# Kernel optimization log

Hardware: AMD Instinct MI355X
Metric: run time of the kernel (lower is better)

The kernel has to match this reference:

```python
import jax, jax.numpy as jnp
import numpy as np

NEG_SLOPE = 0.2  # LeakyReLU slope
B, F_BAND, T = 32, 128, 2048
HID, NCLASS = 256, 64


def _corrcoef(m):
    # m: [..., n, k] -> correlation matrix between rows, [..., n, n] (torch.corrcoef semantics)
    m = m - m.mean(axis=-1, keepdims=True)
    c = jnp.einsum('...ik,...jk->...ij', m, m)
    d = jnp.sqrt(jnp.clip(jnp.diagonal(c, axis1=-2, axis2=-1), 0.0, None))
    corr = c / (d[..., :, None] * d[..., None, :])
    return jnp.clip(corr, -1.0, 1.0)


def _leaky(x):
    return jnp.where(x >= 0, x, NEG_SLOPE * x)


def setup_inputs() -> dict:
    key = jax.random.key(0)
    ks = jax.random.split(key, 9)
    def lin(k, fin, fout):
        return jax.random.normal(k, (fin, fout), dtype=jnp.float32) / np.sqrt(fin)
    x = jax.random.normal(ks[0], (B, F_BAND, T), dtype=jnp.float32)
    return {
        'x': x,
        'W1': lin(ks[1], T, HID),      'b1': jnp.zeros((HID,), jnp.float32),
        'W2': lin(ks[2], HID, HID),    'b2': jnp.zeros((HID,), jnp.float32),
        'W3': lin(ks[3], HID, NCLASS), 'b3': jnp.zeros((NCLASS,), jnp.float32),
        'W4': lin(ks[4], NCLASS, NCLASS), 'b4': jnp.zeros((NCLASS,), jnp.float32),
    }


def reference(x, W1, b1, W2, b2, W3, b3, W4, b4):
    Bs, Fb, Tt = x.shape
    node = Fb
    step = node  # typeFeature=2 -> overlap=0
    A = len(range(0, Tt - node, step))  # number of time windows
    # windows: x[:, :, a*node:(a+1)*node] -> [B, A, F, node]
    xw = x[:, :, :A * node].reshape(Bs, Fb, A, node).transpose(0, 2, 1, 3)
    # torch.corrcoef(fi.T): rows = window-column index (node), variables over F bands
    adj = _corrcoef(jnp.swapaxes(xw, -1, -2))  # [B, A, node, node] == [B, A, F, F]
    adj = jnp.nan_to_num((adj + 1.0) * 0.5)
    # gnnBlock vectorized over all A windows (x broadcast along A). Dropout is eval-mode no-op.
    h = _leaky(jnp.einsum('banm,bmt->bant', adj, x) @ W1 + b1)    # [B,A,F,HID]
    h = _leaky(jnp.einsum('banm,bamh->banh', adj, h) @ W2 + b2)   # [B,A,F,HID]
    xa = _leaky(jnp.einsum('banm,bamh->banh', adj, h) @ W3 + b3)  # [B,A,F,C]
    # typeFeature==2 head: mean over nodes, corrcoef over windows, gc4
    xa = xa.mean(axis=2)         # [B, A, C]
    adj2 = _corrcoef(xa)         # [B, A, A]
    out = _leaky(jnp.einsum('bij,bjc->bic', adj2, xa) @ W4 + b4)  # [B, A, C]
    # max over dim=1; GradMultiply with grad_mul=1.0 is identity in fwd
    return out.max(axis=1)       # [B, C]
```

## Files before the change

### kernel.cpp

```cpp
#include <hip/hip_runtime.h>


typedef float f32x4 __attribute__((ext_vector_type(4)));
typedef __bf16 bf16x8 __attribute__((ext_vector_type(8)));
typedef unsigned short u16x4 __attribute__((ext_vector_type(4)));
typedef unsigned short u16x8 __attribute__((ext_vector_type(8)));

__device__ inline unsigned short f2b(float f) {
  unsigned int u = __float_as_uint(f);
  unsigned int r = u + 0x7fffu + ((u >> 16) & 1u);
  return (unsigned short)(r >> 16);
}
__device__ inline float leaky(float v) { return v >= 0.f ? v : 0.2f * v; }

#define SWZ(k, r) ((k) ^ (((r) & 7) << 3))

__global__ __launch_bounds__(256) void k_prep(const float* __restrict__ x,
                                              const float* __restrict__ W1,
                                              const float* __restrict__ W2,
                                              const float* __restrict__ W3,
                                              unsigned short* __restrict__ W1T,
                                              unsigned short* __restrict__ W2T,
                                              unsigned short* __restrict__ W3T,
                                              unsigned short* __restrict__ xT) {
  __shared__ float t[64][65];
  const int bid = blockIdx.x;
  const int tid = threadIdx.x;
  if (bid < 148) {
    const float* src;
    unsigned short* dst;
    int K, N, k0, n0;
    if (bid < 128) {
      src = W1; dst = W1T; K = 2048; N = 256;
      k0 = (bid >> 2) * 64; n0 = (bid & 3) * 64;
    } else if (bid < 144) {
      src = W2; dst = W2T; K = 256; N = 256;
      int i = bid - 128; k0 = (i >> 2) * 64; n0 = (i & 3) * 64;
    } else {
      src = W3; dst = W3T; K = 256; N = 64;
      int i = bid - 144; k0 = i * 64; n0 = 0;
    }
#pragma unroll
    for (int it = 0; it < 16; ++it) {
      int e = tid + it * 256, r = e >> 6, c = e & 63;
      t[r][c] = src[(size_t)(k0 + r) * N + n0 + c];
    }
    __syncthreads();
#pragma unroll
    for (int it = 0; it < 16; ++it) {
      int e = tid + it * 256, rr = e >> 6, cc = e & 63;
      dst[(size_t)(n0 + rr) * K + k0 + cc] = f2b(t[cc][rr]);
    }
  } else {
    int idx = bid - 148;
    int b = idx >> 6, rem = idx & 63;
    int tt = rem >> 1, ft = rem & 1;
    int t0 = tt * 64, f0 = ft * 64;
    const float* xb = x + ((size_t)b * 128 + f0) * 2048 + t0;
#pragma unroll
    for (int it = 0; it < 16; ++it) {
      int e = tid + it * 256, r = e >> 6, c = e & 63;
      t[r][c] = xb[(size_t)r * 2048 + c];
    }
    __syncthreads();
    unsigned short* dst = xT + ((size_t)b * 2048 + t0) * 128 + f0;
#pragma unroll
    for (int it = 0; it < 4; ++it) {
      int e = tid + it * 256, rr = e >> 4, c4 = (e & 15) * 4;
      u16x4 s;
#pragma unroll
      for (int q = 0; q < 4; ++q) s[q] = f2b(t[c4 + q][rr]);
      *(u16x4*)&dst[rr * 128 + c4] = s;
    }
  }
}

__global__ __launch_bounds__(512) void k_xw1(const float* __restrict__ x,
                                             const unsigned short* __restrict__ W1T,
                                             unsigned short* __restrict__ XW1T) {
  __shared__ __align__(16) unsigned short sX[2][64 * 64];
  const int tid = threadIdx.x;
  const int w = tid >> 6, lane = tid & 63;
  const int l15 = lane & 15, l4 = lane >> 4;
  const int bx = blockIdx.x;
  const int hid0 = (bx >> 1) * 64, f0 = (bx & 1) * 64;
  const int b = blockIdx.y;
  const float* xb = x + ((size_t)b * 128 + f0) * 2048;
  const int arow = hid0 + (w & 3) * 16 + l15;
  const int nb = (w >> 2) * 32;
  const int fr = tid >> 3, k8 = (tid & 7) * 8;

  f32x4 xr2[2];
  f32x4 acc[2] = {};

  auto LOADX = [&](int kb) {
    xr2[0] = *(const f32x4*)&xb[(size_t)fr * 2048 + kb * 64 + k8];
    xr2[1] = *(const f32x4*)&xb[(size_t)fr * 2048 + kb * 64 + k8 + 4];
  };
  auto STOREX = [&](int buf) {
    u16x8 s;
#pragma unroll
    for (int j = 0; j < 8; ++j) s[j] = f2b(xr2[j >> 2][j & 3]);
    *(u16x8*)&sX[buf][fr * 64 + SWZ(k8, fr)] = s;
  };

  LOADX(0);
  STOREX(0);
  __syncthreads();
  for (int kb = 0; kb < 32; ++kb) {
    if (kb < 31) LOADX(kb + 1);
    const int buf = kb & 1;
    bf16x8 af0 = *(const bf16x8*)&W1T[(size_t)arow * 2048 + kb * 64 + l4 * 8];
    bf16x8 af1 = *(const bf16x8*)&W1T[(size_t)arow * 2048 + kb * 64 + 32 + l4 * 8];
#pragma unroll
    for (int nt = 0; nt < 2; ++nt) {
      int br = nb + nt * 16 + l15;
      bf16x8 b0 = *(const bf16x8*)&sX[buf][br * 64 + SWZ(l4 * 8, br)];
      acc[nt] = __builtin_amdgcn_mfma_f32_16x16x32_bf16(af0, b0, acc[nt], 0, 0, 0);
    }
#pragma unroll
    for (int nt = 0; nt < 2; ++nt) {
      int br = nb + nt * 16 + l15;
      bf16x8 b1 = *(const bf16x8*)&sX[buf][br * 64 + SWZ(32 + l4 * 8, br)];
      acc[nt] = __builtin_amdgcn_mfma_f32_16x16x32_bf16(af1, b1, acc[nt], 0, 0, 0);
    }
    if (kb < 31) {
      STOREX(buf ^ 1);
      __syncthreads();
    }
  }
  unsigned short* dst = XW1T + (size_t)b * 256 * 128;
#pragma unroll
  for (int nt = 0; nt < 2; ++nt)
#pragma unroll
    for (int r = 0; r < 4; ++r) {
      int p = hid0 + (w & 3) * 16 + l4 * 4 + r;
      int f = f0 + nb + nt * 16 + l15;
      dst[p * 128 + f] = f2b(acc[nt][r]);
    }
}

__global__ __launch_bounds__(512, 4) void k_chain(
    const unsigned short* __restrict__ xT, const unsigned short* __restrict__ XW1T,
    const unsigned short* __restrict__ W2T, const unsigned short* __restrict__ W3T,
    const float* __restrict__ b1g, const float* __restrict__ b2g,
    const float* __restrict__ b3g, float* __restrict__ gXa) {
  __shared__ __align__(16) unsigned short R0[128 * 128];
  __shared__ __align__(16) unsigned short R1[128 * 128];
  __shared__ float fS[384];

  const int tid = threadIdx.x;
  const int w = tid >> 6, lane = tid & 63;
  const int l15 = lane & 15, l4 = lane >> 4;
  const int b = blockIdx.x / 15, a = blockIdx.x % 15;
  const int m0 = w * 16;

  const unsigned short* src = xT + ((size_t)b * 2048 + (size_t)a * 128) * 128;
#pragma unroll
  for (int it = 0; it < 4; ++it) {
    int tt = tid + it * 512;
    int j = tt >> 4, f8 = (tt & 15) * 8;
    *(u16x8*)&R1[j * 128 + SWZ(f8, j)] = *(const u16x8*)&src[j * 128 + f8];
  }
  __syncthreads();

  {
    f32x4 acc8[8] = {};
    f32x4 sacc = {};
    bf16x8 ones;
#pragma unroll
    for (int q = 0; q < 8; ++q) ones[q] = (__bf16)1.0f;
    __builtin_amdgcn_s_setprio(1);
#pragma unroll
    for (int ks = 0; ks < 4; ++ks) {
      int ar = m0 + l15;
      bf16x8 af = *(const bf16x8*)&R1[ar * 128 + SWZ(ks * 32 + l4 * 8, ar)];
      sacc = __builtin_amdgcn_mfma_f32_16x16x32_bf16(af, ones, sacc, 0, 0, 0);
#pragma unroll
      for (int nt = 0; nt < 8; ++nt) {
        int br = nt * 16 + l15;
        bf16x8 bf = *(const bf16x8*)&R1[br * 128 + SWZ(ks * 32 + l4 * 8, br)];
        acc8[nt] = __builtin_amdgcn_mfma_f32_16x16x32_bf16(af, bf, acc8[nt], 0, 0, 0);
      }
    }
    __builtin_amdgcn_s_setprio(0);
    if (l15 == 0) {
#pragma unroll
      for (int r = 0; r < 4; ++r) fS[m0 + l4 * 4 + r] = sacc[r];
    }
    __syncthreads();
    const float inv128 = 1.f / 128.f;
    float fcol[8];
#pragma unroll
    for (int nt = 0; nt < 8; ++nt) fcol[nt] = fS[nt * 16 + l15];
#pragma unroll
    for (int nt = 0; nt < 8; ++nt)
#pragma unroll
      for (int r = 0; r < 4; ++r) {
        int row = m0 + l4 * 4 + r, col = nt * 16 + l15;
        float c = acc8[nt][r] - sacc[r] * fcol[nt] * inv128;
        acc8[nt][r] = c;
        if (row == col) fS[128 + row] = c;
      }
    __syncthreads();
    if (tid < 128) {
      float d = fS[128 + tid];
      fS[256 + tid] = d > 0.f ? 1.f / sqrtf(d) : 0.f;
    }
    __syncthreads();
    float djv[8], div[4];
#pragma unroll
    for (int nt = 0; nt < 8; ++nt) djv[nt] = fS[256 + nt * 16 + l15];
#pragma unroll
    for (int r = 0; r < 4; ++r) div[r] = fS[256 + m0 + l4 * 4 + r];
#pragma unroll
    for (int nt = 0; nt < 8; ++nt)
#pragma unroll
      for (int r = 0; r < 4; ++r) {
        int row = m0 + l4 * 4 + r, col = nt * 16 + l15;
        float v = acc8[nt][r] * div[r] * djv[nt];
        v = fminf(1.f, fmaxf(-1.f, v));
        v = 0.5f * v + 0.5f;
        if (div[r] == 0.f || djv[nt] == 0.f) v = 0.f;
        R0[row * 128 + SWZ(col, row)] = f2b(v);
      }
  }
  bf16x8 afj[4];
#pragma unroll
  for (int ks = 0; ks < 4; ++ks)
    afj[ks] = *(const bf16x8*)&R0[(m0 + l15) * 128 + SWZ(ks * 32 + l4 * 8, m0 + l15)];
  __syncthreads();

  const unsigned short* XWb = XW1T + (size_t)b * 256 * 128;
#pragma unroll 1
  for (int half = 0; half < 2; ++half) {
    f32x4 acc[8] = {};
    __builtin_amdgcn_s_setprio(1);
#pragma unroll
    for (int ks = 0; ks < 4; ++ks)
#pragma unroll
      for (int nt = 0; nt < 8; ++nt) {
        bf16x8 bf = *(const bf16x8*)&XWb[(size_t)(half * 128 + nt * 16 + l15) * 128 + ks * 32 + l4 * 8];
        acc[nt] = __builtin_amdgcn_mfma_f32_16x16x32_bf16(afj[ks], bf, acc[nt], 0, 0, 0);
      }
    __builtin_amdgcn_s_setprio(0);
    unsigned short* Rd = half ? R1 : R0;
#pragma unroll
    for (int nt = 0; nt < 8; ++nt) {
      float bias = b1g[half * 128 + nt * 16 + l15];
#pragma unroll
      for (int r = 0; r < 4; ++r) {
        int row = m0 + l4 * 4 + r, col = nt * 16 + l15;
        Rd[row * 128 + SWZ(col, row)] = f2b(leaky(acc[nt][r] + bias));
      }
    }
  }
  __syncthreads();

  {
    f32x4 u2[2][8] = {};
    __builtin_amdgcn_s_setprio(1);
#pragma unroll
    for (int ks = 0; ks < 8; ++ks) {
      bf16x8 a0 = *(const bf16x8*)&W2T[(size_t)(w * 32 + l15) * 256 + ks * 32 + l4 * 8];
      bf16x8 a1 = *(const bf16x8*)&W2T[(size_t)(w * 32 + 16 + l15) * 256 + ks * 32 + l4 * 8];
      const unsigned short* Rs = (ks < 4) ? R0 : R1;
      int kk = (ks & 3) * 32 + l4 * 8;
#pragma unroll
      for (int nt = 0; nt < 8; ++nt) {
        int br = nt * 16 + l15;
        bf16x8 bf = *(const bf16x8*)&Rs[br * 128 + SWZ(kk, br)];
        u2[0][nt] = __builtin_amdgcn_mfma_f32_16x16x32_bf16(a0, bf, u2[0][nt], 0, 0, 0);
        u2[1][nt] = __builtin_amdgcn_mfma_f32_16x16x32_bf16(a1, bf, u2[1][nt], 0, 0, 0);
      }
    }
    __builtin_amdgcn_s_setprio(0);
    __syncthreads();
#pragma unroll
    for (int mt = 0; mt < 2; ++mt)
#pragma unroll
      for (int nt = 0; nt < 8; ++nt)
#pragma unroll
        for (int r = 0; r < 4; ++r) {
          int grow = w * 32 + mt * 16 + l4 * 4 + r;
          int col = nt * 16 + l15;
          unsigned short* Rd = (grow < 128) ? R0 : R1;
          int lr = grow & 127;
          Rd[lr * 128 + SWZ(col, lr)] = f2b(u2[mt][nt][r]);
        }
  }
  __syncthreads();

  f32x4 h2acc[8];
#pragma unroll
  for (int nt = 0; nt < 8; ++nt) h2acc[nt] = f32x4{0.f, 0.f, 0.f, 0.f};
  __builtin_amdgcn_s_setprio(1);
#pragma unroll
  for (int ks = 0; ks < 4; ++ks)
#pragma unroll
    for (int nt = 0; nt < 8; ++nt) {
      int br = nt * 16 + l15;
      bf16x8 bf = *(const bf16x8*)&R0[br * 128 + SWZ(ks * 32 + l4 * 8, br)];
      h2acc[nt] = __builtin_amdgcn_mfma_f32_16x16x32_bf16(afj[ks], bf, h2acc[nt], 0, 0, 0);
    }
  __builtin_amdgcn_s_setprio(0);
  __syncthreads();
#pragma unroll
  for (int nt = 0; nt < 8; ++nt) {
    float bias = b2g[nt * 16 + l15];
#pragma unroll
    for (int r = 0; r < 4; ++r) {
      int row = m0 + l4 * 4 + r, col = nt * 16 + l15;
      R0[row * 128 + SWZ(col, row)] = f2b(leaky(h2acc[nt][r] + bias));
    }
  }
  __syncthreads();

  f32x4 u3[4] = {};
  const int mrow = (w >> 1) * 16, ntb = (w & 1) * 4;
  __builtin_amdgcn_s_setprio(1);
#pragma unroll
  for (int ks = 0; ks < 4; ++ks) {
    bf16x8 a3 = *(const bf16x8*)&W3T[(size_t)(mrow + l15) * 256 + ks * 32 + l4 * 8];
#pragma unroll
    for (int nti = 0; nti < 4; ++nti) {
      int br = (ntb + nti) * 16 + l15;
      bf16x8 bf = *(const bf16x8*)&R0[br * 128 + SWZ(ks * 32 + l4 * 8, br)];
      u3[nti] = __builtin_amdgcn_mfma_f32_16x16x32_bf16(a3, bf, u3[nti], 0, 0, 0);
    }
  }
#pragma unroll
  for (int nt = 0; nt < 8; ++nt) h2acc[nt] = f32x4{0.f, 0.f, 0.f, 0.f};
#pragma unroll
  for (int ks = 0; ks < 4; ++ks)
#pragma unroll
    for (int nt = 0; nt < 8; ++nt) {
      int br = nt * 16 + l15;
      bf16x8 bf = *(const bf16x8*)&R1[br * 128 + SWZ(ks * 32 + l4 * 8, br)];
      h2acc[nt] = __builtin_amdgcn_mfma_f32_16x16x32_bf16(afj[ks], bf, h2acc[nt], 0, 0, 0);
    }
  __builtin_amdgcn_s_setprio(0);
  __syncthreads();
#pragma unroll
  for (int nt = 0; nt < 8; ++nt) {
    float bias = b2g[128 + nt * 16 + l15];
#pragma unroll
    for (int r = 0; r < 4; ++r) {
      int row = m0 + l4 * 4 + r, col = nt * 16 + l15;
      R1[row * 128 + SWZ(col, row)] = f2b(leaky(h2acc[nt][r] + bias));
    }
  }
  __syncthreads();

  __builtin_amdgcn_s_setprio(1);
#pragma unroll
  for (int ks = 0; ks < 4; ++ks) {
    bf16x8 a3 = *(const bf16x8*)&W3T[(size_t)(mrow + l15) * 256 + 128 + ks * 32 + l4 * 8];
#pragma unroll
    for (int nti = 0; nti < 4; ++nti) {
      int br = (ntb + nti) * 16 + l15;
      bf16x8 bf = *(const bf16x8*)&R1[br * 128 + SWZ(ks * 32 + l4 * 8, br)];
      u3[nti] = __builtin_amdgcn_mfma_f32_16x16x32_bf16(a3, bf, u3[nti], 0, 0, 0);
    }
  }
  __builtin_amdgcn_s_setprio(0);
  __syncthreads();
#pragma unroll
  for (int nti = 0; nti < 4; ++nti)
#pragma unroll
    for (int r = 0; r < 4; ++r) {
      int grow = mrow + l4 * 4 + r;
      int col = (ntb + nti) * 16 + l15;
      R0[grow * 128 + SWZ(col, grow)] = f2b(u3[nti][r]);
    }
  __syncthreads();

  {
    f32x4 xacc[4] = {};
    __builtin_amdgcn_s_setprio(1);
#pragma unroll
    for (int ks = 0; ks < 4; ++ks)
#pragma unroll
      for (int nt = 0; nt < 4; ++nt) {
        int br = nt * 16 + l15;
        bf16x8 bf = *(const bf16x8*)&R0[br * 128 + SWZ(ks * 32 + l4 * 8, br)];
        xacc[nt] = __builtin_amdgcn_mfma_f32_16x16x32_bf16(afj[ks], bf, xacc[nt], 0, 0, 0);
      }
    __builtin_amdgcn_s_setprio(0);
    float* xaf = reinterpret_cast<float*>(R1);
#pragma unroll
    for (int nt = 0; nt < 4; ++nt) {
      float bias = b3g[nt * 16 + l15];
#pragma unroll
      for (int r = 0; r < 4; ++r) {
        int row = m0 + l4 * 4 + r, col = nt * 16 + l15;
        xaf[row * 64 + col] = leaky(xacc[nt][r] + bias);
      }
    }
  }
  __syncthreads();
  {
    const float* xaf = reinterpret_cast<const float*>(R1);
    float* part = reinterpret_cast<float*>(R0);
    int c = tid & 63, g = tid >> 6;
    float s = 0.f;
#pragma unroll
    for (int i = 0; i < 16; ++i) s += xaf[(g * 16 + i) * 64 + c];
    part[g * 64 + c] = s;
    __syncthreads();
    if (tid < 64) {
      float tt = 0.f;
#pragma unroll
      for (int gg = 0; gg < 8; ++gg) tt += part[gg * 64 + tid];
      gXa[((size_t)b * 15 + a) * 64 + tid] = tt * (1.f / 128.f);
    }
  }
}

__global__ __launch_bounds__(256) void k_head(const float* __restrict__ gXa,
                                              const float* __restrict__ W4,
                                              const float* __restrict__ b4,
                                              float* __restrict__ out) {
  __shared__ float xb[15 * 64];
  __shared__ float c2[15 * 16];
  __shared__ float mu[15];
  __shared__ float dinv[15];
  __shared__ float yy[15 * 64];
  __shared__ float zz[15 * 64];
  const int b = blockIdx.x;
  const int tid = threadIdx.x;
  for (int e = tid; e < 960; e += 256) xb[e] = gXa[(size_t)b * 960 + e];
  __syncthreads();
  if (tid < 15) {
    float s = 0.f;
    for (int c = 0; c < 64; ++c) s += xb[tid * 64 + c];
    mu[tid] = s * (1.f / 64.f);
  }
  __syncthreads();
  if (tid < 225) {
    int p = tid / 15, q = tid % 15;
    float s = 0.f;
    for (int c = 0; c < 64; ++c)
      s += (xb[p * 64 + c] - mu[p]) * (xb[q * 64 + c] - mu[q]);
    c2[p * 16 + q] = s;
  }
  __syncthreads();
  if (tid < 15) {
    float d = c2[tid * 16 + tid];
    dinv[tid] = d > 0.f ? (1.f / sqrtf(d)) : 0.f;
  }
  __syncthreads();
  if (tid < 225) {
    int p = tid / 15, q = tid % 15;
    float v = c2[p * 16 + q] * dinv[p] * dinv[q];
    v = fminf(1.f, fmaxf(-1.f, v));
    if (dinv[p] == 0.f || dinv[q] == 0.f) v = 0.f;
    c2[p * 16 + q] = v;
  }
  __syncthreads();
  for (int e = tid; e < 960; e += 256) {
    int p = e >> 6, c = e & 63;
    float s = 0.f;
    for (int q = 0; q < 15; ++q) s += c2[p * 16 + q] * xb[q * 64 + c];
    yy[e] = s;
  }
  __syncthreads();
  for (int e = tid; e < 960; e += 256) {
    int p = e >> 6, c = e & 63;
    float s = b4[c];
    for (int k = 0; k < 64; ++k) s += yy[p * 64 + k] * W4[k * 64 + c];
    zz[e] = leaky(s);
  }
  __syncthreads();
  if (tid < 64) {
    float m = -INFINITY;
    for (int p = 0; p < 15; ++p) m = fmaxf(m, zz[p * 64 + tid]);
    out[(size_t)b * 64 + tid] = m;
  }
}

extern "C" void kernel_launch(void* const* d_in, const int* in_sizes, int n_in,
                              void* d_out, int out_size, void* d_ws, size_t ws_size,
                              hipStream_t stream) {
  const float* x  = (const float*)d_in[0];
  const float* W1 = (const float*)d_in[1];
  const float* b1 = (const float*)d_in[2];
  const float* W2 = (const float*)d_in[3];
  const float* b2 = (const float*)d_in[4];
  const float* W3 = (const float*)d_in[5];
  const float* b3 = (const float*)d_in[6];
  const float* W4 = (const float*)d_in[7];
  const float* b4 = (const float*)d_in[8];
  float* out = (float*)d_out;

  char* ws = (char*)d_ws;
  unsigned short* xT   = (unsigned short*)ws;
  unsigned short* XW1T = (unsigned short*)(ws + 16777216);
  unsigned short* W1T  = (unsigned short*)(ws + 18874368);
  unsigned short* W2T  = (unsigned short*)(ws + 19922944);
  unsigned short* W3T  = (unsigned short*)(ws + 20054016);
  float* gXa           = (float*)(ws + 20086784);

  k_prep<<<2196, 256, 0, stream>>>(x, W1, W2, W3, W1T, W2T, W3T, xT);
  dim3 gx(8, 32);
  k_xw1<<<gx, 512, 0, stream>>>(x, W1T, XW1T);
  k_chain<<<480, 512, 0, stream>>>(xT, XW1T, W2T, W3T, b1, b2, b3, gXa);
  k_head<<<32, 256, 0, stream>>>(gXa, W4, b4, out);
}
```

Baseline: 132.8 us.

## Fuse x transpose with XW1 GEMM, stage XW1 in LDS, reorder chain stages

```diff
diff --git a/kernel.cpp b/kernel.cpp
--- a/kernel.cpp
+++ b/kernel.cpp
@@ -3,7 +3,6 @@
 
 typedef float f32x4 __attribute__((ext_vector_type(4)));
 typedef __bf16 bf16x8 __attribute__((ext_vector_type(8)));
-typedef unsigned short u16x4 __attribute__((ext_vector_type(4)));
 typedef unsigned short u16x8 __attribute__((ext_vector_type(8)));
 
 __device__ inline unsigned short f2b(float f) {
@@ -15,129 +14,121 @@
 
 #define SWZ(k, r) ((k) ^ (((r) & 7) << 3))
 
-__global__ __launch_bounds__(256) void k_prep(const float* __restrict__ x,
-                                              const float* __restrict__ W1,
-                                              const float* __restrict__ W2,
-                                              const float* __restrict__ W3,
-                                              unsigned short* __restrict__ W1T,
-                                              unsigned short* __restrict__ W2T,
-                                              unsigned short* __restrict__ W3T,
-                                              unsigned short* __restrict__ xT) {
+__global__ __launch_bounds__(256) void k_prepw(const float* __restrict__ W1,
+                                               const float* __restrict__ W2,
+                                               const float* __restrict__ W3,
+                                               unsigned short* __restrict__ W1T,
+                                               unsigned short* __restrict__ W2T,
+                                               unsigned short* __restrict__ W3T) {
   __shared__ float t[64][65];
   const int bid = blockIdx.x;
   const int tid = threadIdx.x;
-  if (bid < 148) {
-    const float* src;
-    unsigned short* dst;
-    int K, N, k0, n0;
-    if (bid < 128) {
-      src = W1; dst = W1T; K = 2048; N = 256;
-      k0 = (bid >> 2) * 64; n0 = (bid & 3) * 64;
-    } else if (bid < 144) {
-      src = W2; dst = W2T; K = 256; N = 256;
-      int i = bid - 128; k0 = (i >> 2) * 64; n0 = (i & 3) * 64;
-    } else {
-      src = W3; dst = W3T; K = 256; N = 64;
-      int i = bid - 144; k0 = i * 64; n0 = 0;
-    }
-#pragma unroll
-    for (int it = 0; it < 16; ++it) {
-      int e = tid + it * 256, r = e >> 6, c = e & 63;
-      t[r][c] = src[(size_t)(k0 + r) * N + n0 + c];
-    }
+  const float* src;
+  unsigned short* dst;
+  int K, N, k0, n0;
+  if (bid < 128) {
+    src = W1; dst = W1T; K = 2048; N = 256;
+    k0 = (bid >> 2) * 64; n0 = (bid & 3) * 64;
+  } else if (bid < 144) {
+    src = W2; dst = W2T; K = 256; N = 256;
+    int i = bid - 128; k0 = (i >> 2) * 64; n0 = (i & 3) * 64;
+  } else {
+    src = W3; dst = W3T; K = 256; N = 64;
+    int i = bid - 144; k0 = i * 64; n0 = 0;
+  }
+#pragma unroll
+  for (int it = 0; it < 16; ++it) {
+    int e = tid + it * 256, r = e >> 6, c = e & 63;
+    t[r][c] = src[(size_t)(k0 + r) * N + n0 + c];
+  }
+  __syncthreads();
+#pragma unroll
+  for (int it = 0; it < 16; ++it) {
+    int e = tid + it * 256, rr = e >> 6, cc = e & 63;
+    dst[(size_t)(n0 + rr) * K + k0 + cc] = f2b(t[cc][rr]);
+  }
+}
+
+__global__ __launch_bounds__(512) void k_front(const float* __restrict__ x,
+                                               const unsigned short* __restrict__ W1T,
+                                               unsigned short* __restrict__ xT,
+                                               unsigned short* __restrict__ XW1T) {
+  __shared__ __align__(16) char ldsbuf[16896];
+  const int bid = blockIdx.x;
+  const int tid = threadIdx.x;
+  if (bid < 2048) {
+    float (*t)[65] = reinterpret_cast<float (*)[65]>(ldsbuf);
+    int b = bid >> 6, rem = bid & 63;
+    int t0 = (rem >> 1) * 64, f0 = (rem & 1) * 64;
+    const float* xb = x + ((size_t)b * 128 + f0) * 2048 + t0;
+    int r = tid >> 3, c8 = (tid & 7) * 8;
+    f32x4 v0 = *(const f32x4*)&xb[(size_t)r * 2048 + c8];
+    f32x4 v1 = *(const f32x4*)&xb[(size_t)r * 2048 + c8 + 4];
+    *(f32x4*)&t[r][c8] = v0;
+    *(f32x4*)&t[r][c8 + 4] = v1;
     __syncthreads();
-#pragma unroll
-    for (int it = 0; it < 16; ++it) {
-      int e = tid + it * 256, rr = e >> 6, cc = e & 63;
-      dst[(size_t)(n0 + rr) * K + k0 + cc] = f2b(t[cc][rr]);
-    }
+    u16x8 s;
+#pragma unroll
+    for (int q = 0; q < 8; ++q) s[q] = f2b(t[c8 + q][r]);
+    *(u16x8*)&xT[((size_t)b * 2048 + t0 + r) * 128 + f0 + c8] = s;
   } else {
-    int idx = bid - 148;
-    int b = idx >> 6, rem = idx & 63;
-    int tt = rem >> 1, ft = rem & 1;
-    int t0 = tt * 64, f0 = ft * 64;
-    const float* xb = x + ((size_t)b * 128 + f0) * 2048 + t0;
-#pragma unroll
-    for (int it = 0; it < 16; ++it) {
-      int e = tid + it * 256, r = e >> 6, c = e & 63;
-      t[r][c] = xb[(size_t)r * 2048 + c];
-    }
+    unsigned short (*sX)[64 * 64] = reinterpret_cast<unsigned short (*)[64 * 64]>(ldsbuf);
+    const int i = bid - 2048;
+    const int b = i >> 1, f0 = (i & 1) * 64;
+    const int w = tid >> 6, lane = tid & 63;
+    const int l15 = lane & 15, l4 = lane >> 4;
+    const float* xb = x + ((size_t)b * 128 + f0) * 2048;
+    const int fr = tid >> 3, k8 = (tid & 7) * 8;
+    f32x4 xr0, xr1;
+    f32x4 acc[2][4] = {};
+
+    auto LOADX = [&](int kb) {
+      xr0 = *(const f32x4*)&xb[(size_t)fr * 2048 + kb * 64 + k8];
+      xr1 = *(const f32x4*)&xb[(size_t)fr * 2048 + kb * 64 + k8 + 4];
+    };
+    auto STOREX = [&](int buf) {
+      u16x8 s;
+#pragma unroll
+      for (int q = 0; q < 8; ++q) s[q] = f2b(q < 4 ? xr0[q] : xr1[q - 4]);
+      *(u16x8*)&sX[buf][fr * 64 + SWZ(k8, fr)] = s;
+    };
+
+    LOADX(0);
+    STOREX(0);
     __syncthreads();
-    unsigned short* dst = xT + ((size_t)b * 2048 + t0) * 128 + f0;
-#pragma unroll
-    for (int it = 0; it < 4; ++it) {
-      int e = tid + it * 256, rr = e >> 4, c4 = (e & 15) * 4;
-      u16x4 s;
-#pragma unroll
-      for (int q = 0; q < 4; ++q) s[q] = f2b(t[c4 + q][rr]);
-      *(u16x4*)&dst[rr * 128 + c4] = s;
-    }
-  }
-}
-
-__global__ __launch_bounds__(512) void k_xw1(const float* __restrict__ x,
-                                             const unsigned short* __restrict__ W1T,
-                                             unsigned short* __restrict__ XW1T) {
-  __shared__ __align__(16) unsigned short sX[2][64 * 64];
-  const int tid = threadIdx.x;
-  const int w = tid >> 6, lane = tid & 63;
-  const int l15 = lane & 15, l4 = lane >> 4;
-  const int bx = blockIdx.x;
-  const int hid0 = (bx >> 1) * 64, f0 = (bx & 1) * 64;
-  const int b = blockIdx.y;
-  const float* xb = x + ((size_t)b * 128 + f0) * 2048;
-  const int arow = hid0 + (w & 3) * 16 + l15;
-  const int nb = (w >> 2) * 32;
-  const int fr = tid >> 3, k8 = (tid & 7) * 8;
-
-  f32x4 xr2[2];
-  f32x4 acc[2] = {};
-
-  auto LOADX = [&](int kb) {
-    xr2[0] = *(const f32x4*)&xb[(size_t)fr * 2048 + kb * 64 + k8];
-    xr2[1] = *(const f32x4*)&xb[(size_t)fr * 2048 + kb * 64 + k8 + 4];
-  };
-  auto STOREX = [&](int buf) {
-    u16x8 s;
-#pragma unroll
-    for (int j = 0; j < 8; ++j) s[j] = f2b(xr2[j >> 2][j & 3]);
-    *(u16x8*)&sX[buf][fr * 64 + SWZ(k8, fr)] = s;
-  };
-
-  LOADX(0);
-  STOREX(0);
-  __syncthreads();
-  for (int kb = 0; kb < 32; ++kb) {
-    if (kb < 31) LOADX(kb + 1);
-    const int buf = kb & 1;
-    bf16x8 af0 = *(const bf16x8*)&W1T[(size_t)arow * 2048 + kb * 64 + l4 * 8];
-    bf16x8 af1 = *(const bf16x8*)&W1T[(size_t)arow * 2048 + kb * 64 + 32 + l4 * 8];
-#pragma unroll
-    for (int nt = 0; nt < 2; ++nt) {
-      int br = nb + nt * 16 + l15;
-      bf16x8 b0 = *(const bf16x8*)&sX[buf][br * 64 + SWZ(l4 * 8, br)];
-      acc[nt] = __builtin_amdgcn_mfma_f32_16x16x32_bf16(af0, b0, acc[nt], 0, 0, 0);
-    }
-#pragma unroll
-    for (int nt = 0; nt < 2; ++nt) {
-      int br = nb + nt * 16 + l15;
-      bf16x8 b1 = *(const bf16x8*)&sX[buf][br * 64 + SWZ(32 + l4 * 8, br)];
-      acc[nt] = __builtin_amdgcn_mfma_f32_16x16x32_bf16(af1, b1, acc[nt], 0, 0, 0);
-    }
-    if (kb < 31) {
-      STOREX(buf ^ 1);
-      __syncthreads();
-    }
-  }
-  unsigned short* dst = XW1T + (size_t)b * 256 * 128;
-#pragma unroll
-  for (int nt = 0; nt < 2; ++nt)
-#pragma unroll
-    for (int r = 0; r < 4; ++r) {
-      int p = hid0 + (w & 3) * 16 + l4 * 4 + r;
-      int f = f0 + nb + nt * 16 + l15;
-      dst[p * 128 + f] = f2b(acc[nt][r]);
-    }
+    for (int kb = 0; kb < 32; ++kb) {
+      if (kb < 31) LOADX(kb + 1);
+      const int buf = kb & 1;
+#pragma unroll
+      for (int ks = 0; ks < 2; ++ks) {
+        bf16x8 af[2];
+#pragma unroll
+        for (int mt = 0; mt < 2; ++mt)
+          af[mt] = *(const bf16x8*)&W1T[(size_t)(w * 32 + mt * 16 + l15) * 2048 + kb * 64 + ks * 32 + l4 * 8];
+#pragma unroll
+        for (int nt = 0; nt < 4; ++nt) {
+          int br = nt * 16 + l15;
+          bf16x8 bf = *(const bf16x8*)&sX[buf][br * 64 + SWZ(ks * 32 + l4 * 8, br)];
+#pragma unroll
+          for (int mt = 0; mt < 2; ++mt)
+            acc[mt][nt] = __builtin_amdgcn_mfma_f32_16x16x32_bf16(af[mt], bf, acc[mt][nt], 0, 0, 0);
+        }
+      }
+      if (kb < 31) {
+        STOREX(buf ^ 1);
+        __syncthreads();
+      }
+    }
+#pragma unroll
+    for (int mt = 0; mt < 2; ++mt)
+#pragma unroll
+      for (int nt = 0; nt < 4; ++nt)
+#pragma unroll
+        for (int r = 0; r < 4; ++r) {
+          int p = w * 32 + mt * 16 + l4 * 4 + r;
+          XW1T[((size_t)b * 256 + p) * 128 + f0 + nt * 16 + l15] = f2b(acc[mt][nt][r]);
+        }
+  }
 }
 
 __global__ __launch_bounds__(512, 4) void k_chain(
@@ -152,8 +143,20 @@
   const int tid = threadIdx.x;
   const int w = tid >> 6, lane = tid & 63;
   const int l15 = lane & 15, l4 = lane >> 4;
-  const int b = blockIdx.x / 15, a = blockIdx.x % 15;
+  const int ridx = (blockIdx.x & 7) * 60 + (blockIdx.x >> 3);
+  const int b = ridx / 15, a = ridx % 15;
   const int m0 = w * 16;
+  const unsigned short* XWb = XW1T + (size_t)b * 256 * 128;
+
+  u16x8 st0[4];
+  int srow[4], sn8[4];
+#pragma unroll
+  for (int q = 0; q < 4; ++q) {
+    int c = q * 512 + tid;
+    srow[q] = c >> 4;
+    sn8[q] = (c & 15) * 8;
+    st0[q] = *(const u16x8*)&XWb[srow[q] * 128 + sn8[q]];
+  }
 
   const unsigned short* src = xT + ((size_t)b * 2048 + (size_t)a * 128) * 128;
 #pragma unroll
@@ -231,87 +234,142 @@
     afj[ks] = *(const bf16x8*)&R0[(m0 + l15) * 128 + SWZ(ks * 32 + l4 * 8, m0 + l15)];
   __syncthreads();
 
-  const unsigned short* XWb = XW1T + (size_t)b * 256 * 128;
-#pragma unroll 1
-  for (int half = 0; half < 2; ++half) {
+#pragma unroll
+  for (int q = 0; q < 4; ++q)
+    *(u16x8*)&R0[srow[q] * 128 + SWZ(sn8[q], srow[q])] = st0[q];
+  u16x8 st1[4];
+#pragma unroll
+  for (int q = 0; q < 4; ++q)
+    st1[q] = *(const u16x8*)&XWb[(128 + srow[q]) * 128 + sn8[q]];
+  __syncthreads();
+
+  {
     f32x4 acc[8] = {};
     __builtin_amdgcn_s_setprio(1);
 #pragma unroll
     for (int ks = 0; ks < 4; ++ks)
 #pragma unroll
       for (int nt = 0; nt < 8; ++nt) {
-        bf16x8 bf = *(const bf16x8*)&XWb[(size_t)(half * 128 + nt * 16 + l15) * 128 + ks * 32 + l4 * 8];
+        int br = nt * 16 + l15;
+        bf16x8 bf = *(const bf16x8*)&R0[br * 128 + SWZ(ks * 32 + l4 * 8, br)];
         acc[nt] = __builtin_amdgcn_mfma_f32_16x16x32_bf16(afj[ks], bf, acc[nt], 0, 0, 0);
       }
     __builtin_amdgcn_s_setprio(0);
-    unsigned short* Rd = half ? R1 : R0;
 #pragma unroll
     for (int nt = 0; nt < 8; ++nt) {
-      float bias = b1g[half * 128 + nt * 16 + l15];
+      float bias = b1g[nt * 16 + l15];
 #pragma unroll
       for (int r = 0; r < 4; ++r) {
         int row = m0 + l4 * 4 + r, col = nt * 16 + l15;
-        Rd[row * 128 + SWZ(col, row)] = f2b(leaky(acc[nt][r] + bias));
-      }
-    }
-  }
-  __syncthreads();
-
+        R1[row * 128 + SWZ(col, row)] = f2b(leaky(acc[nt][r] + bias));
+      }
+    }
+  }
+  __syncthreads();
+
+  f32x4 u2[2][8] = {};
   {
-    f32x4 u2[2][8] = {};
+#pragma unroll
+    for (int q = 0; q < 4; ++q)
+      *(u16x8*)&R0[srow[q] * 128 + SWZ(sn8[q], srow[q])] = st1[q];
     __builtin_amdgcn_s_setprio(1);
 #pragma unroll
-    for (int ks = 0; ks < 8; ++ks) {
+    for (int ks = 0; ks < 4; ++ks) {
       bf16x8 a0 = *(const bf16x8*)&W2T[(size_t)(w * 32 + l15) * 256 + ks * 32 + l4 * 8];
       bf16x8 a1 = *(const bf16x8*)&W2T[(size_t)(w * 32 + 16 + l15) * 256 + ks * 32 + l4 * 8];
-      const unsigned short* Rs = (ks < 4) ? R0 : R1;
-      int kk = (ks & 3) * 32 + l4 * 8;
 #pragma unroll
       for (int nt = 0; nt < 8; ++nt) {
         int br = nt * 16 + l15;
-        bf16x8 bf = *(const bf16x8*)&Rs[br * 128 + SWZ(kk, br)];
+        bf16x8 bf = *(const bf16x8*)&R1[br * 128 + SWZ(ks * 32 + l4 * 8, br)];
         u2[0][nt] = __builtin_amdgcn_mfma_f32_16x16x32_bf16(a0, bf, u2[0][nt], 0, 0, 0);
         u2[1][nt] = __builtin_amdgcn_mfma_f32_16x16x32_bf16(a1, bf, u2[1][nt], 0, 0, 0);
       }
     }
     __builtin_amdgcn_s_setprio(0);
-    __syncthreads();
-#pragma unroll
-    for (int mt = 0; mt < 2; ++mt)
-#pragma unroll
-      for (int nt = 0; nt < 8; ++nt)
-#pragma unroll
-        for (int r = 0; r < 4; ++r) {
-          int grow = w * 32 + mt * 16 + l4 * 4 + r;
-          int col = nt * 16 + l15;
-          unsigned short* Rd = (grow < 128) ? R0 : R1;
-          int lr = grow & 127;
-          Rd[lr * 128 + SWZ(col, lr)] = f2b(u2[mt][nt][r]);
-        }
-  }
-  __syncthreads();
-
-  f32x4 h2acc[8];
-#pragma unroll
-  for (int nt = 0; nt < 8; ++nt) h2acc[nt] = f32x4{0.f, 0.f, 0.f, 0.f};
+  }
+  __syncthreads();
+
+  {
+    f32x4 acc[8] = {};
+    __builtin_amdgcn_s_setprio(1);
+#pragma unroll
+    for (int ks = 0; ks < 4; ++ks)
+#pragma unroll
+      for (int nt = 0; nt < 8; ++nt) {
+        int br = nt * 16 + l15;
+        bf16x8 bf = *(const bf16x8*)&R0[br * 128 + SWZ(ks * 32 + l4 * 8, br)];
+        acc[nt] = __builtin_amdgcn_mfma_f32_16x16x32_bf16(afj[ks], bf, acc[nt], 0, 0, 0);
+      }
+    __builtin_amdgcn_s_setprio(0);
+#pragma unroll
+    for (int nt = 0; nt < 8; ++nt) {
+      float bias = b1g[128 + nt * 16 + l15];
+#pragma unroll
+      for (int r = 0; r < 4; ++r) {
+        int row = m0 + l4 * 4 + r, col = nt * 16 + l15;
+        R1[row * 128 + SWZ(col, row)] = f2b(leaky(acc[nt][r] + bias));
+      }
+    }
+  }
+  __syncthreads();
+
+  {
+    __builtin_amdgcn_s_setprio(1);
+#pragma unroll
+    for (int ks = 0; ks < 4; ++ks) {
+      bf16x8 a0 = *(const bf16x8*)&W2T[(size_t)(w * 32 + l15) * 256 + 128 + ks * 32 + l4 * 8];
+      bf16x8 a1 = *(const bf16x8*)&W2T[(size_t)(w * 32 + 16 + l15) * 256 + 128 + ks * 32 + l4 * 8];
+#pragma unroll
+      for (int nt = 0; nt < 8; ++nt) {
+        int br = nt * 16 + l15;
+        bf16x8 bf = *(const bf16x8*)&R1[br * 128 + SWZ(ks * 32 + l4 * 8, br)];
+        u2[0][nt] = __builtin_amdgcn_mfma_f32_16x16x32_bf16(a0, bf, u2[0][nt], 0, 0, 0);
+        u2[1][nt] = __builtin_amdgcn_mfma_f32_16x16x32_bf16(a1, bf, u2[1][nt], 0, 0, 0);
+      }
+    }
+    __builtin_amdgcn_s_setprio(0);
+  }
+  __syncthreads();
+
+#pragma unroll
+  for (int mt = 0; mt < 2; ++mt)
+#pragma unroll
+    for (int nt = 0; nt < 8; ++nt)
+#pragma unroll
+      for (int r = 0; r < 4; ++r) {
+        int grow = w * 32 + mt * 16 + l4 * 4 + r;
+        int col = nt * 16 + l15;
+        unsigned short* Rd = (grow < 128) ? R0 : R1;
+        int lr = grow & 127;
+        Rd[lr * 128 + SWZ(col, lr)] = f2b(u2[mt][nt][r]);
+      }
+  __syncthreads();
+
+  f32x4 h2acc[16];
+#pragma unroll
+  for (int nt = 0; nt < 16; ++nt) h2acc[nt] = f32x4{0.f, 0.f, 0.f, 0.f};
   __builtin_amdgcn_s_setprio(1);
 #pragma unroll
   for (int ks = 0; ks < 4; ++ks)
 #pragma unroll
-    for (int nt = 0; nt < 8; ++nt) {
-      int br = nt * 16 + l15;
-      bf16x8 bf = *(const bf16x8*)&R0[br * 128 + SWZ(ks * 32 + l4 * 8, br)];
+    for (int nt = 0; nt < 16; ++nt) {
+      int brl = (nt & 7) * 16 + l15;
+      const unsigned short* Rs = (nt < 8) ? R0 : R1;
+      bf16x8 bf = *(const bf16x8*)&Rs[brl * 128 + SWZ(ks * 32 + l4 * 8, brl)];
       h2acc[nt] = __builtin_amdgcn_mfma_f32_16x16x32_bf16(afj[ks], bf, h2acc[nt], 0, 0, 0);
     }
   __builtin_amdgcn_s_setprio(0);
   __syncthreads();
-#pragma unroll
-  for (int nt = 0; nt < 8; ++nt) {
+
+#pragma unroll
+  for (int nt = 0; nt < 16; ++nt) {
     float bias = b2g[nt * 16 + l15];
 #pragma unroll
     for (int r = 0; r < 4; ++r) {
-      int row = m0 + l4 * 4 + r, col = nt * 16 + l15;
-      R0[row * 128 + SWZ(col, row)] = f2b(leaky(h2acc[nt][r] + bias));
+      int row = m0 + l4 * 4 + r;
+      int coll = (nt & 7) * 16 + l15;
+      unsigned short* Rd = (nt < 8) ? R0 : R1;
+      Rd[row * 128 + SWZ(coll, row)] = f2b(leaky(h2acc[nt][r] + bias));
     }
   }
   __syncthreads();
@@ -320,51 +378,22 @@
   const int mrow = (w >> 1) * 16, ntb = (w & 1) * 4;
   __builtin_amdgcn_s_setprio(1);
 #pragma unroll
-  for (int ks = 0; ks < 4; ++ks) {
-    bf16x8 a3 = *(const bf16x8*)&W3T[(size_t)(mrow + l15) * 256 + ks * 32 + l4 * 8];
-#pragma unroll
-    for (int nti = 0; nti < 4; ++nti) {
-      int br = (ntb + nti) * 16 + l15;
-      bf16x8 bf = *(const bf16x8*)&R0[br * 128 + SWZ(ks * 32 + l4 * 8, br)];
-      u3[nti] = __builtin_amdgcn_mfma_f32_16x16x32_bf16(a3, bf, u3[nti], 0, 0, 0);
-    }
-  }
-#pragma unroll
-  for (int nt = 0; nt < 8; ++nt) h2acc[nt] = f32x4{0.f, 0.f, 0.f, 0.f};
-#pragma unroll
-  for (int ks = 0; ks < 4; ++ks)
-#pragma unroll
-    for (int nt = 0; nt < 8; ++nt) {
-      int br = nt * 16 + l15;
-      bf16x8 bf = *(const bf16x8*)&R1[br * 128 + SWZ(ks * 32 + l4 * 8, br)];
-      h2acc[nt] = __builtin_amdgcn_mfma_f32_16x16x32_bf16(afj[ks], bf, h2acc[nt], 0, 0, 0);
-    }
+  for (int kh = 0; kh < 2; ++kh) {
+    const unsigned short* Rs = kh ? R1 : R0;
+#pragma unroll
+    for (int ks = 0; ks < 4; ++ks) {
+      bf16x8 a3 = *(const bf16x8*)&W3T[(size_t)(mrow + l15) * 256 + kh * 128 + ks * 32 + l4 * 8];
+#pragma unroll
+      for (int nti = 0; nti < 4; ++nti) {
+        int br = (ntb + nti) * 16 + l15;
+        bf16x8 bf = *(const bf16x8*)&Rs[br * 128 + SWZ(ks * 32 + l4 * 8, br)];
+        u3[nti] = __builtin_amdgcn_mfma_f32_16x16x32_bf16(a3, bf, u3[nti], 0, 0, 0);
+      }
+    }
+  }
   __builtin_amdgcn_s_setprio(0);
   __syncthreads();
-#pragma unroll
-  for (int nt = 0; nt < 8; ++nt) {
-    float bias = b2g[128 + nt * 16 + l15];
-#pragma unroll
-    for (int r = 0; r < 4; ++r) {
-      int row = m0 + l4 * 4 + r, col = nt * 16 + l15;
-      R1[row * 128 + SWZ(col, row)] = f2b(leaky(h2acc[nt][r] + bias));
-    }
-  }
-  __syncthreads();
-
-  __builtin_amdgcn_s_setprio(1);
-#pragma unroll
-  for (int ks = 0; ks < 4; ++ks) {
-    bf16x8 a3 = *(const bf16x8*)&W3T[(size_t)(mrow + l15) * 256 + 128 + ks * 32 + l4 * 8];
-#pragma unroll
-    for (int nti = 0; nti < 4; ++nti) {
-      int br = (ntb + nti) * 16 + l15;
-      bf16x8 bf = *(const bf16x8*)&R1[br * 128 + SWZ(ks * 32 + l4 * 8, br)];
-      u3[nti] = __builtin_amdgcn_mfma_f32_16x16x32_bf16(a3, bf, u3[nti], 0, 0, 0);
-    }
-  }
-  __builtin_amdgcn_s_setprio(0);
-  __syncthreads();
+
 #pragma unroll
   for (int nti = 0; nti < 4; ++nti)
 #pragma unroll
@@ -387,33 +416,25 @@
         xacc[nt] = __builtin_amdgcn_mfma_f32_16x16x32_bf16(afj[ks], bf, xacc[nt], 0, 0, 0);
       }
     __builtin_amdgcn_s_setprio(0);
-    float* xaf = reinterpret_cast<float*>(R1);
+    float* pf = reinterpret_cast<float*>(R1);
 #pragma unroll
     for (int nt = 0; nt < 4; ++nt) {
       float bias = b3g[nt * 16 + l15];
-#pragma unroll
-      for (int r = 0; r < 4; ++r) {
-        int row = m0 + l4 * 4 + r, col = nt * 16 + l15;
-        xaf[row * 64 + col] = leaky(xacc[nt][r] + bias);
-      }
-    }
-  }
-  __syncthreads();
-  {
-    const float* xaf = reinterpret_cast<const float*>(R1);
-    float* part = reinterpret_cast<float*>(R0);
-    int c = tid & 63, g = tid >> 6;
+      float v = 0.f;
+#pragma unroll
+      for (int r = 0; r < 4; ++r) v += leaky(xacc[nt][r] + bias);
+      v += __shfl_xor(v, 16);
+      v += __shfl_xor(v, 32);
+      if (l4 == 0) pf[w * 64 + nt * 16 + l15] = v;
+    }
+  }
+  __syncthreads();
+  if (tid < 64) {
+    const float* pf = reinterpret_cast<const float*>(R1);
     float s = 0.f;
 #pragma unroll
-    for (int i = 0; i < 16; ++i) s += xaf[(g * 16 + i) * 64 + c];
-    part[g * 64 + c] = s;
-    __syncthreads();
-    if (tid < 64) {
-      float tt = 0.f;
-#pragma unroll
-      for (int gg = 0; gg < 8; ++gg) tt += part[gg * 64 + tid];
-      gXa[((size_t)b * 15 + a) * 64 + tid] = tt * (1.f / 128.f);
-    }
+    for (int gg = 0; gg < 8; ++gg) s += pf[gg * 64 + tid];
+    gXa[((size_t)b * 15 + a) * 64 + tid] = s * (1.f / 128.f);
   }
 }
 
@@ -501,9 +522,8 @@
   unsigned short* W3T  = (unsigned short*)(ws + 20054016);
   float* gXa           = (float*)(ws + 20086784);
 
-  k_prep<<<2196, 256, 0, stream>>>(x, W1, W2, W3, W1T, W2T, W3T, xT);
-  dim3 gx(8, 32);
-  k_xw1<<<gx, 512, 0, stream>>>(x, W1T, XW1T);
+  k_prepw<<<148, 256, 0, stream>>>(W1, W2, W3, W1T, W2T, W3T);
+  k_front<<<2112, 512, 0, stream>>>(x, W1T, xT, XW1T);
   k_chain<<<480, 512, 0, stream>>>(xT, XW1T, W2T, W3T, b1, b2, b3, gXa);
   k_head<<<32, 256, 0, stream>>>(gXa, W4, b4, out);
 }
```

Result: slower. 138.7 us (+4.4%).
